# Optimization experiments

Hardware: AMD Instinct MI355X
Metric: run time of the kernel (lower is better)

The kernel has to match this reference:

```python
import jax, jax.numpy as jnp
import numpy as np


def setup_inputs() -> dict:
    key = jax.random.key(0)
    b, h, w = 16, 32, 32
    correlation_tensor = jax.random.normal(key, (b, h * w, h, w), dtype=jnp.float32)
    return {"correlation_tensor": correlation_tensor}


def reference(correlation_tensor):
    # out[b, a, c, i, j] = resized[b, a-(h-1)+i, c-(w-1)+j, i, j] (0 where out of range)
    b, hw, h, w = correlation_tensor.shape
    resized = correlation_tensor.reshape(b, h, w, h, w)
    H, W = 2 * h - 1, 2 * w - 1

    a = jnp.arange(H)[:, None]          # [H,1]
    i = jnp.arange(h)[None, :]          # [1,h]
    p = a - (h - 1) + i                 # [H,h] source row index
    p_valid = (p >= 0) & (p < h)
    p_clip = jnp.clip(p, 0, h - 1)

    c = jnp.arange(W)[:, None]          # [W,1]
    j = jnp.arange(w)[None, :]          # [1,w]
    q = c - (w - 1) + j                 # [W,w] source col index
    q_valid = (q >= 0) & (q < w)
    q_clip = jnp.clip(q, 0, w - 1)

    # Gather: indices broadcast over [H, W, h, w]
    out = resized[:,
                  p_clip[:, None, :, None],            # [H,1,h,1]
                  q_clip[None, :, None, :],            # [1,W,1,w]
                  jnp.arange(h)[None, None, :, None],  # [1,1,h,1]
                  jnp.arange(w)[None, None, None, :]]  # [1,1,1,w]
    mask = p_valid[:, None, :, None] & q_valid[None, :, None, :]  # [H,W,h,w]
    out = jnp.where(mask[None], out, jnp.zeros((), dtype=out.dtype))
    return out.reshape(b, H * W, h, w)
```

## Files before the change

### kernel.cpp

```cpp
#include <hip/hip_runtime.h>


#define LDSS 33

__global__ __launch_bounds__(256) void CorrelationAlign_kernel(
    const float* __restrict__ in, float* __restrict__ out) {
  __shared__ float tile[32 * LDSS];

  const int bid = blockIdx.x;
  const int L = (bid & 7) * (16 * 63 * 32 / 8) + (bid >> 3);

  const int i  = L & 31;
  const int ba = L >> 5;
  const int a  = ba % 63;
  const int b  = ba / 63;
  const int p  = a + i - 31;
  const int t  = threadIdx.x;

  float* outbase = out + (size_t)(b * 3969 + a * 63) * 1024 + i * 32;

  if ((unsigned)p < 32u) {
    const float* inbase = in + (size_t)(b * 1024 + p * 32) * 1024 + i * 32;
    {
      const int q  = t >> 3;
      const int j0 = (t & 7) * 4;
      const float4 v =
          *reinterpret_cast<const float4*>(inbase + (size_t)q * 1024 + j0);
      float* row = &tile[q * LDSS + j0];
      row[0] = v.x; row[1] = v.y; row[2] = v.z; row[3] = v.w;
    }
    __syncthreads();

    for (int task = t; task < 63 * 8; task += 256) {
      const int c  = task >> 3;
      const int j0 = (task & 7) * 4;
      float4 v;
      float* vp = reinterpret_cast<float*>(&v);
#pragma unroll
      for (int k = 0; k < 4; ++k) {
        const int j = j0 + k;
        const int q = c + j - 31;
        vp[k] = ((unsigned)q < 32u) ? tile[q * LDSS + j] : 0.0f;
      }
      *reinterpret_cast<float4*>(outbase + (size_t)c * 1024 + j0) = v;
    }
  } else {
    const float4 z = make_float4(0.f, 0.f, 0.f, 0.f);
    for (int task = t; task < 63 * 8; task += 256) {
      const int c  = task >> 3;
      const int j0 = (task & 7) * 4;
      *reinterpret_cast<float4*>(outbase + (size_t)c * 1024 + j0) = z;
    }
  }
}

extern "C" void kernel_launch(void* const* d_in, const int* in_sizes, int n_in,
                              void* d_out, int out_size, void* d_ws,
                              size_t ws_size, hipStream_t stream) {
  (void)in_sizes; (void)n_in; (void)out_size; (void)d_ws; (void)ws_size;
  const float* in = (const float*)d_in[0];
  float* out = (float*)d_out;
  const int grid = 16 * 63 * 32;
  CorrelationAlign_kernel<<<grid, 256, 0, stream>>>(in, out);
}
```

Baseline: 65.40 us.

## Process eight source rows per block for contiguous 1KB output stores

Each block now handles eight consecutive i rows instead of one, so the grid shrinks eightfold. Each block stages eight 32x32 input tiles in LDS and writes contiguous 1 KB output segments per c, where the old code wrote 128-byte pieces. The aim is fewer blocks, less launch and scheduling overhead, and better-coalesced stores. The cost is larger LDS use per block, which may lower occupancy, and the removal of the old block-index swizzle that spread work across XCDs.

```diff
diff --git a/kernel.cpp b/kernel.cpp
--- a/kernel.cpp
+++ b/kernel.cpp
@@ -1,55 +1,63 @@
 #include <hip/hip_runtime.h>
 
 
-#define LDSS 33
+#define TSTR 1057
 
 __global__ __launch_bounds__(256) void CorrelationAlign_kernel(
     const float* __restrict__ in, float* __restrict__ out) {
-  __shared__ float tile[32 * LDSS];
+  __shared__ float tile[8 * TSTR];
 
   const int bid = blockIdx.x;
-  const int L = (bid & 7) * (16 * 63 * 32 / 8) + (bid >> 3);
-
-  const int i  = L & 31;
-  const int ba = L >> 5;
+  const int g  = bid & 3;
+  const int ba = bid >> 2;
   const int a  = ba % 63;
   const int b  = ba / 63;
-  const int p  = a + i - 31;
+  const int i0 = g * 8;
   const int t  = threadIdx.x;
 
-  float* outbase = out + (size_t)(b * 3969 + a * 63) * 1024 + i * 32;
+  float* outbase = out + (size_t)(b * 3969 + a * 63) * 1024 + i0 * 32;
+  const int plo = a + i0 - 31;
 
-  if ((unsigned)p < 32u) {
-    const float* inbase = in + (size_t)(b * 1024 + p * 32) * 1024 + i * 32;
-    {
-      const int q  = t >> 3;
-      const int j0 = (t & 7) * 4;
-      const float4 v =
-          *reinterpret_cast<const float4*>(inbase + (size_t)q * 1024 + j0);
-      float* row = &tile[q * LDSS + j0];
-      row[0] = v.x; row[1] = v.y; row[2] = v.z; row[3] = v.w;
+  if (plo <= 31 && plo + 7 >= 0) {
+    const int q  = t >> 3;
+    const int j0 = (t & 7) * 4;
+#pragma unroll
+    for (int it = 0; it < 8; ++it) {
+      const int p = plo + it;
+      if ((unsigned)p < 32u) {
+        const float4 v = *reinterpret_cast<const float4*>(
+            in + (size_t)(b * 1024 + p * 32 + q) * 1024 + (i0 + it) * 32 + j0);
+        float* dst = &tile[it * TSTR + q * 33 + j0];
+        dst[0] = v.x; dst[1] = v.y; dst[2] = v.z; dst[3] = v.w;
+      }
     }
     __syncthreads();
 
-    for (int task = t; task < 63 * 8; task += 256) {
-      const int c  = task >> 3;
-      const int j0 = (task & 7) * 4;
+    for (int task = t; task < 63 * 64; task += 256) {
+      const int c   = task >> 6;
+      const int l   = task & 63;
+      const int isb = l >> 3;
+      const int js  = (l & 7) * 4;
+      const int p   = plo + isb;
+      const bool pv = (unsigned)p < 32u;
       float4 v;
       float* vp = reinterpret_cast<float*>(&v);
 #pragma unroll
       for (int k = 0; k < 4; ++k) {
-        const int j = j0 + k;
-        const int q = c + j - 31;
-        vp[k] = ((unsigned)q < 32u) ? tile[q * LDSS + j] : 0.0f;
+        const int j  = js + k;
+        const int qq = c + j - 31;
+        const int qc = min(max(qq, 0), 31);
+        const float x = tile[isb * TSTR + qc * 33 + j];
+        vp[k] = (pv && (unsigned)qq < 32u) ? x : 0.0f;
       }
-      *reinterpret_cast<float4*>(outbase + (size_t)c * 1024 + j0) = v;
+      *reinterpret_cast<float4*>(outbase + (size_t)c * 1024 + l * 4) = v;
     }
   } else {
     const float4 z = make_float4(0.f, 0.f, 0.f, 0.f);
-    for (int task = t; task < 63 * 8; task += 256) {
-      const int c  = task >> 3;
-      const int j0 = (task & 7) * 4;
-      *reinterpret_cast<float4*>(outbase + (size_t)c * 1024 + j0) = z;
+    for (int task = t; task < 63 * 64; task += 256) {
+      const int c = task >> 6;
+      const int l = task & 63;
+      *reinterpret_cast<float4*>(outbase + (size_t)c * 1024 + l * 4) = z;
     }
   }
 }
@@ -60,6 +68,6 @@
   (void)in_sizes; (void)n_in; (void)out_size; (void)d_ws; (void)ws_size;
   const float* in = (const float*)d_in[0];
   float* out = (float*)d_out;
-  const int grid = 16 * 63 * 32;
+  const int grid = 16 * 63 * 4;
   CorrelationAlign_kernel<<<grid, 256, 0, stream>>>(in, out);
 }
```

Measured after the change: 83.60 us. 1.28x slower.

## Map one wavefront per output tile and drop block-level barrier

Applied to the files above, without the earlier changes.

Each 64-lane wavefront now handles one (b,a,i) tile with its own LDS slice, so a 256-thread block covers four tiles and the grid shrinks fourfold. The __syncthreads is removed because each wave only reads LDS it wrote itself, and the loops are fully unrolled with clamped LDS indices so the loads can be issued unconditionally. The old bid&7 block-swizzle is dropped, which changes the order in which output memory is written, and LDS use per block grows fourfold.

```diff
diff --git a/kernel.cpp b/kernel.cpp
--- a/kernel.cpp
+++ b/kernel.cpp
@@ -1,55 +1,63 @@
 #include <hip/hip_runtime.h>
 
 
-#define LDSS 33
+#define WLDS (32 * 33)
 
 __global__ __launch_bounds__(256) void CorrelationAlign_kernel(
     const float* __restrict__ in, float* __restrict__ out) {
-  __shared__ float tile[32 * LDSS];
+  __shared__ float lds[4 * WLDS];
 
-  const int bid = blockIdx.x;
-  const int L = (bid & 7) * (16 * 63 * 32 / 8) + (bid >> 3);
-
-  const int i  = L & 31;
-  const int ba = L >> 5;
+  const int t    = threadIdx.x;
+  const int w    = t >> 6;
+  const int lane = t & 63;
+  const int gw   = blockIdx.x * 4 + w;
+  const int i  = gw & 31;
+  const int ba = gw >> 5;
   const int a  = ba % 63;
   const int b  = ba / 63;
   const int p  = a + i - 31;
-  const int t  = threadIdx.x;
 
+  float* tile = &lds[w * WLDS];
   float* outbase = out + (size_t)(b * 3969 + a * 63) * 1024 + i * 32;
+
+  const int rj0 = (lane & 7) * 4;
+  const int rq  = lane >> 3;
 
   if ((unsigned)p < 32u) {
     const float* inbase = in + (size_t)(b * 1024 + p * 32) * 1024 + i * 32;
-    {
-      const int q  = t >> 3;
-      const int j0 = (t & 7) * 4;
+#pragma unroll
+    for (int r = 0; r < 4; ++r) {
+      const int q = r * 8 + rq;
       const float4 v =
-          *reinterpret_cast<const float4*>(inbase + (size_t)q * 1024 + j0);
-      float* row = &tile[q * LDSS + j0];
-      row[0] = v.x; row[1] = v.y; row[2] = v.z; row[3] = v.w;
+          *reinterpret_cast<const float4*>(inbase + (size_t)q * 1024 + rj0);
+      float* dst = &tile[q * 33 + rj0];
+      dst[0] = v.x; dst[1] = v.y; dst[2] = v.z; dst[3] = v.w;
     }
-    __syncthreads();
 
-    for (int task = t; task < 63 * 8; task += 256) {
-      const int c  = task >> 3;
-      const int j0 = (task & 7) * 4;
-      float4 v;
-      float* vp = reinterpret_cast<float*>(&v);
 #pragma unroll
-      for (int k = 0; k < 4; ++k) {
-        const int j = j0 + k;
-        const int q = c + j - 31;
-        vp[k] = ((unsigned)q < 32u) ? tile[q * LDSS + j] : 0.0f;
+    for (int s = 0; s < 8; ++s) {
+      const int c = s * 8 + rq;
+      if (c < 63) {
+        float4 v;
+        float* vp = reinterpret_cast<float*>(&v);
+#pragma unroll
+        for (int k = 0; k < 4; ++k) {
+          const int j  = rj0 + k;
+          const int q  = c + j - 31;
+          const int qc = min(max(q, 0), 31);
+          const float x = tile[qc * 33 + j];
+          vp[k] = ((unsigned)q < 32u) ? x : 0.0f;
+        }
+        *reinterpret_cast<float4*>(outbase + (size_t)c * 1024 + rj0) = v;
       }
-      *reinterpret_cast<float4*>(outbase + (size_t)c * 1024 + j0) = v;
     }
   } else {
     const float4 z = make_float4(0.f, 0.f, 0.f, 0.f);
-    for (int task = t; task < 63 * 8; task += 256) {
-      const int c  = task >> 3;
-      const int j0 = (task & 7) * 4;
-      *reinterpret_cast<float4*>(outbase + (size_t)c * 1024 + j0) = z;
+#pragma unroll
+    for (int s = 0; s < 8; ++s) {
+      const int c = s * 8 + rq;
+      if (c < 63)
+        *reinterpret_cast<float4*>(outbase + (size_t)c * 1024 + rj0) = z;
     }
   }
 }
@@ -60,6 +68,6 @@
   (void)in_sizes; (void)n_in; (void)out_size; (void)d_ws; (void)ws_size;
   const float* in = (const float*)d_in[0];
   float* out = (float*)d_out;
-  const int grid = 16 * 63 * 32;
+  const int grid = 16 * 63 * 32 / 4;
   CorrelationAlign_kernel<<<grid, 256, 0, stream>>>(in, out);
 }
```

Result: faster. 60.28 us (-7.8%).
